# Kernel tuning notes

Hardware: AMD Instinct MI355X
Metric: run time of the kernel (lower is better)

Reference implementation:

```python
import jax, jax.numpy as jnp
import numpy as np

B, N, D, H = 32, 64, 256, 256
WORD_NUM, REL_NUM, POS_NUM, CAT_NUM = 50000, 50, 48, 5


def setup_inputs() -> dict:
    key = jax.random.key(0)
    ks = jax.random.split(key, 20)
    rng = np.random.default_rng(0)
    # valid dependency trees: head[i] < i, head[0] = -1 (root)
    heads_np = np.zeros((B, N), dtype=np.int32)
    for b in range(B):
        heads_np[b, 0] = -1
        for i in range(1, N):
            heads_np[b, i] = rng.integers(0, i)
    p = lambda k, shape: (0.02 * jax.random.normal(k, shape)).astype(jnp.float32)
    z = lambda shape: jnp.zeros(shape, jnp.float32)
    return {
        "xs": jax.random.randint(ks[0], (B, N), 0, WORD_NUM),
        "heads": jnp.asarray(heads_np),
        "rels": jax.random.randint(ks[1], (B, N), 0, REL_NUM),
        "labels": jax.random.randint(ks[2], (B, N), 0, WORD_NUM),
        "poss": jax.random.randint(ks[3], (B, N), 0, POS_NUM),
        "xlengths": jnp.full((B,), N, dtype=jnp.int32),
        "target_start": jnp.zeros((B,), jnp.int32),
        "target_end": jnp.full((B,), N - 1, jnp.int32),
        "x_mask": jnp.ones((B, N), jnp.float32),
        # parameters
        "emb_W": p(ks[4], (WORD_NUM, D)),
        "rel_W": p(ks[5], (REL_NUM, D)),
        "gru_Wi_f": p(ks[6], (2 * D, 3 * H)), "gru_Wh_f": p(ks[7], (H, 3 * H)),
        "gru_bi_f": z((3 * H,)), "gru_bh_f": z((3 * H,)),
        "gru_Wi_b": p(ks[8], (2 * D, 3 * H)), "gru_Wh_b": p(ks[9], (H, 3 * H)),
        "gru_bi_b": z((3 * H,)), "gru_bh_b": z((3 * H,)),
        "Wt": p(ks[10], (2 * H, D)), "bt": z((D,)),
        "dt_Wx": p(ks[11], (2 * D, 3 * H)), "dt_Uh": p(ks[12], (H, 3 * H)), "dt_b": z((3 * H,)),
        "td_Wx": p(ks[13], (2 * D, 3 * H)), "td_Uh": p(ks[14], (H, 3 * H)), "td_b": z((3 * H,)),
        "fc_W": p(ks[15], (2 * H, 100)), "fc_b": z((100,)),
        "fc2_W": p(ks[16], (100, CAT_NUM)), "fc2_b": z((CAT_NUM,)),
    }


def _gru_cell(xpt, hprev, Uh, bh):
    gh = hprev @ Uh + bh
    xr, xz, xn = jnp.split(xpt, 3, axis=-1)
    hr, hz, hn = jnp.split(gh, 3, axis=-1)
    r = jax.nn.sigmoid(xr + hr)
    zg = jax.nn.sigmoid(xz + hz)
    n = jnp.tanh(xn + r * hn)
    return (1.0 - zg) * n + zg * hprev


def _gru_dir(x, Wi, Wh, bi, bh):
    # x: [B,N,2D] -> hidden sequence [B,N,H]
    xp = x @ Wi + bi  # precompute input projections
    def step(h, xpt):
        hnew = _gru_cell(xpt, h, Wh, bh)
        return hnew, hnew
    h0 = jnp.zeros((x.shape[0], Wh.shape[0]), x.dtype)
    _, hs = jax.lax.scan(step, h0, jnp.swapaxes(xp, 0, 1))
    return jnp.swapaxes(hs, 0, 1)


def _dt_tree(inputs, heads, Wx, Uh, b):
    # bottom-up (child-sum) tree GRU; heads[b,i] < i so reversed order is topological
    Bn, Nn, _ = inputs.shape
    Hh = Uh.shape[0]
    xp = inputs @ Wx + b
    bar = jnp.arange(Bn)
    def step(carry, idx):
        C, Hout = carry  # C: accumulated child hidden sums [B,N,H]
        h = _gru_cell(xp[:, idx], C[:, idx], Uh, jnp.zeros((3 * Hh,), inputs.dtype))
        Hout = Hout.at[:, idx].set(h)
        par = heads[:, idx]
        valid = par >= 0
        C = C.at[bar, jnp.where(valid, par, 0)].add(jnp.where(valid[:, None], h, 0.0))
        return (C, Hout), None
    H0 = jnp.zeros((Bn, Nn, Hh), inputs.dtype)
    (_, Hout), _ = jax.lax.scan(step, (H0, H0), jnp.arange(Nn - 1, -1, -1))
    return Hout


def _td_tree(inputs, heads, Wx, Uh, b):
    # top-down tree GRU: parent hidden flows to children; index order 0..N-1 is topological
    Bn, Nn, _ = inputs.shape
    Hh = Uh.shape[0]
    xp = inputs @ Wx + b
    bar = jnp.arange(Bn)
    def step(Hout, idx):
        par = heads[:, idx]
        valid = par >= 0
        hp = jnp.where(valid[:, None], Hout[bar, jnp.where(valid, par, 0)], 0.0)
        h = _gru_cell(xp[:, idx], hp, Uh, jnp.zeros((3 * Hh,), inputs.dtype))
        Hout = Hout.at[:, idx].set(h)
        return Hout, None
    H0 = jnp.zeros((Bn, Nn, Hh), inputs.dtype)
    Hout, _ = jax.lax.scan(step, H0, jnp.arange(Nn))
    return Hout


def reference(xs, heads, rels, labels, poss, xlengths, target_start, target_end, x_mask,
              emb_W, rel_W,
              gru_Wi_f, gru_Wh_f, gru_bi_f, gru_bh_f,
              gru_Wi_b, gru_Wh_b, gru_bi_b, gru_bh_b,
              Wt, bt, dt_Wx, dt_Uh, dt_b, td_Wx, td_Uh, td_b,
              fc_W, fc_b, fc2_W, fc2_b):
    word_emb = emb_W[xs]
    label_emb = emb_W[labels]  # original uses self.embedding for labels too
    emb = jnp.concatenate([word_emb, label_emb], axis=-1)  # [B,N,2D]
    fwd = _gru_dir(emb, gru_Wi_f, gru_Wh_f, gru_bi_f, gru_bh_f)
    bwd = jnp.flip(_gru_dir(jnp.flip(emb, 1), gru_Wi_b, gru_Wh_b, gru_bi_b, gru_bh_b), 1)
    grus = jnp.concatenate([fwd, bwd], axis=-1) @ Wt + bt  # transform -> [B,N,D]
    rel_emb = rel_W[rels]
    outputs = jnp.concatenate([grus, rel_emb], axis=-1)  # [B,N,2D]
    dt_out = _dt_tree(outputs, heads, dt_Wx, dt_Uh, dt_b)
    td_out = _td_tree(outputs, heads, td_Wx, td_Uh, td_b)
    ctx = jnp.concatenate([dt_out, td_out], axis=-1)  # [B,N,2H]
    ctx = jnp.max(ctx, axis=1)  # max_pool1d over length -> [B,2H]
    ctx = ctx @ fc_W + fc_b
    ctx = ctx @ fc2_W + fc2_b
    return ctx
```

## Files before the change

### kernel.cpp

```cpp
#include <hip/hip_runtime.h>


typedef _Float16 half2v __attribute__((ext_vector_type(2)));
typedef _Float16 half8 __attribute__((ext_vector_type(8)));
typedef unsigned int u32x32 __attribute__((ext_vector_type(32)));
typedef float f32x4v __attribute__((ext_vector_type(4)));

__device__ __forceinline__ float fdot2f(unsigned a, unsigned b, float c) {
#if __has_builtin(__builtin_amdgcn_fdot2)
  return __builtin_amdgcn_fdot2(__builtin_bit_cast(half2v, a),
                                __builtin_bit_cast(half2v, b), c, false);
#else
  half2v av = __builtin_bit_cast(half2v, a), bv = __builtin_bit_cast(half2v, b);
  return c + (float)av.x * (float)bv.x + (float)av.y * (float)bv.y;
#endif
}

__device__ __forceinline__ unsigned packh2(float x, float y) {
  half2v p;
  p.x = (_Float16)x;
  p.y = (_Float16)y;
  return __builtin_bit_cast(unsigned, p);
}
__device__ __forceinline__ unsigned short f2u(float x) {
  return __builtin_bit_cast(unsigned short, (_Float16)x);
}
__device__ __forceinline__ float sigm(float x) { return 1.f / (1.f + __expf(-x)); }
__device__ __forceinline__ float tanh_fast(float x) {
  float cx = fminf(fmaxf(x, -15.f), 15.f);
  float e = __expf(2.f * cx);
  return (e - 1.f) / (e + 1.f);
}

__global__ __launch_bounds__(256) void pack_w(const float* __restrict__ W0,
                                              const float* __restrict__ W1,
                                              const float* __restrict__ W2,
                                              const float* __restrict__ W3, unsigned* P0,
                                              unsigned* P1, unsigned* P2, unsigned* P3) {
  const float* W;
  unsigned* P;
  switch (blockIdx.y) {
    case 0: W = W0; P = P0; break;
    case 1: W = W1; P = P1; break;
    case 2: W = W2; P = P2; break;
    default: W = W3; P = P3; break;
  }
  const int tid = blockIdx.x * 256 + threadIdx.x;
  const int i = tid & 3;
  const int u4 = tid >> 2;
  const int jg = u4 & 127;
  const int d4q = u4 >> 7;
  const int d4 = d4q % 48;
  const int q2 = d4q / 48;
  const int col2 = d4 / 24;
  const int rr = d4 % 24;
  const int g = rr >> 3;
  const int p4 = rr & 7;
  const int kp = p4 * 4 + i;
  const int k = q2 * 64 + kp * 2;
  const int col = g * 256 + col2 * 128 + jg;
  P[tid] = packh2(W[(size_t)k * 768 + col], W[(size_t)(k + 1) * 768 + col]);
}

__global__ __launch_bounds__(256) void tsplit2(const float* __restrict__ W0,
                                               const float* __restrict__ W1,
                                               unsigned short* __restrict__ H0,
                                               unsigned short* __restrict__ L0,
                                               unsigned short* __restrict__ H1,
                                               unsigned short* __restrict__ L1, int K,
                                               int N) {
  const float* __restrict__ W = blockIdx.z ? W1 : W0;
  unsigned short* __restrict__ WThi = blockIdx.z ? H1 : H0;
  unsigned short* __restrict__ WTlo = blockIdx.z ? L1 : L0;
  __shared__ float T[32][33];
  const int ky = blockIdx.y * 32, nx = blockIdx.x * 32;
  const int r = threadIdx.x >> 3, c4 = (threadIdx.x & 7) * 4;
  float4 v = *(const float4*)(W + (size_t)(ky + r) * N + nx + c4);
  T[r][c4 + 0] = v.x;
  T[r][c4 + 1] = v.y;
  T[r][c4 + 2] = v.z;
  T[r][c4 + 3] = v.w;
  __syncthreads();
  float f[4] = {T[c4 + 0][r], T[c4 + 1][r], T[c4 + 2][r], T[c4 + 3][r]};
  ushort4 oh, ol;
  {
    _Float16 h0 = (_Float16)f[0], h1 = (_Float16)f[1], h2 = (_Float16)f[2],
             h3 = (_Float16)f[3];
    oh.x = __builtin_bit_cast(unsigned short, h0);
    oh.y = __builtin_bit_cast(unsigned short, h1);
    oh.z = __builtin_bit_cast(unsigned short, h2);
    oh.w = __builtin_bit_cast(unsigned short, h3);
    ol.x = f2u(f[0] - (float)h0);
    ol.y = f2u(f[1] - (float)h1);
    ol.z = f2u(f[2] - (float)h2);
    ol.w = f2u(f[3] - (float)h3);
  }
  *(ushort4*)(WThi + (size_t)(nx + r) * K + ky + c4) = oh;
  *(ushort4*)(WTlo + (size_t)(nx + r) * K + ky + c4) = ol;
}

__global__ void gather_emb_hl(const int* __restrict__ xs, const int* __restrict__ labels,
                              const float* __restrict__ embW,
                              unsigned short* __restrict__ eHi,
                              unsigned short* __restrict__ eLo) {
  const int row = blockIdx.x, t = threadIdx.x;
  const float4* W4 = (const float4*)embW;
  const int src = (t < 64) ? xs[row] : labels[row];
  float4 v = W4[(size_t)src * 64 + (t & 63)];
  float f[4] = {v.x, v.y, v.z, v.w};
  ushort4 oh, ol;
  _Float16 h0 = (_Float16)f[0], h1 = (_Float16)f[1], h2 = (_Float16)f[2],
           h3 = (_Float16)f[3];
  oh.x = __builtin_bit_cast(unsigned short, h0);
  oh.y = __builtin_bit_cast(unsigned short, h1);
  oh.z = __builtin_bit_cast(unsigned short, h2);
// ... 117 lines not shown
        _Float16 h = (_Float16)av[i];
        Ahi[ar][ac8 + i] = h;
        Alo[ar][ac8 + i] = (_Float16)(av[i] - (float)h);
      }
    }
    {
      const float* wp = W + (size_t)(kt + bk) * N + bn + bn8;
      float4 v0 = *(const float4*)wp;
      float4 v1 = *(const float4*)(wp + 4);
      float wv[8] = {v0.x, v0.y, v0.z, v0.w, v1.x, v1.y, v1.z, v1.w};
#pragma unroll
      for (int i = 0; i < 8; ++i) {
        _Float16 h = (_Float16)wv[i];
        Bhi[bn8 + i][bk] = h;
        Blo[bn8 + i][bk] = (_Float16)(wv[i] - (float)h);
      }
    }
    __syncthreads();
    half8 avh = __builtin_bit_cast(half8, *(const uint4*)(&Ahi[fr][fc]));
    half8 avl = __builtin_bit_cast(half8, *(const uint4*)(&Alo[fr][fc]));
#define BH(NT) __builtin_bit_cast(half8, *(const uint4*)(&Bhi[(NT)*16 + lo16][fc]))
#define BL(NT) __builtin_bit_cast(half8, *(const uint4*)(&Blo[(NT)*16 + lo16][fc]))
    half8 b0h = BH(0), b1h = BH(1), b2h = BH(2), b3h = BH(3);
    half8 b0l = BL(0), b1l = BL(1), b2l = BL(2), b3l = BL(3);
#undef BH
#undef BL
    ac0 = __builtin_amdgcn_mfma_f32_16x16x32_f16(avh, b0h, ac0, 0, 0, 0);
    ac1 = __builtin_amdgcn_mfma_f32_16x16x32_f16(avh, b1h, ac1, 0, 0, 0);
    ac2 = __builtin_amdgcn_mfma_f32_16x16x32_f16(avh, b2h, ac2, 0, 0, 0);
    ac3 = __builtin_amdgcn_mfma_f32_16x16x32_f16(avh, b3h, ac3, 0, 0, 0);
    ac0 = __builtin_amdgcn_mfma_f32_16x16x32_f16(avh, b0l, ac0, 0, 0, 0);
    ac1 = __builtin_amdgcn_mfma_f32_16x16x32_f16(avh, b1l, ac1, 0, 0, 0);
    ac2 = __builtin_amdgcn_mfma_f32_16x16x32_f16(avh, b2l, ac2, 0, 0, 0);
    ac3 = __builtin_amdgcn_mfma_f32_16x16x32_f16(avh, b3l, ac3, 0, 0, 0);
    ac0 = __builtin_amdgcn_mfma_f32_16x16x32_f16(avl, b0h, ac0, 0, 0, 0);
    ac1 = __builtin_amdgcn_mfma_f32_16x16x32_f16(avl, b1h, ac1, 0, 0, 0);
    ac2 = __builtin_amdgcn_mfma_f32_16x16x32_f16(avl, b2h, ac2, 0, 0, 0);
    ac3 = __builtin_amdgcn_mfma_f32_16x16x32_f16(avl, b3h, ac3, 0, 0, 0);
    __syncthreads();
  }
  const int hi4 = l >> 4;
#define EPI(AC, NT)                                                            \
  {                                                                            \
    _Pragma("unroll") for (int i = 0; i < 4; ++i) {                            \
      const int row = bm + w * 16 + hi4 * 4 + i;                               \
      const int col = bn + (NT)*16 + lo16;                                     \
      float v = (AC)[i] + bias[col];                                           \
      _Float16 h = (_Float16)v;                                                \
      CHi[(size_t)row * ldc + col] = __builtin_bit_cast(unsigned short, h);    \
      CLo[(size_t)row * ldc + col] = f2u(v - (float)h);                        \
    }                                                                          \
  }
  EPI(ac0, 0) EPI(ac1, 1) EPI(ac2, 2) EPI(ac3, 3)
#undef EPI
}

template <int NP>
__device__ __forceinline__ void stage_w(const uint4* __restrict__ P4, int q2, int jg,
                                        int t, uint2 (*Wl)[512], u32x32& w0, u32x32& w1,
                                        u32x32& w2) {
#pragma unroll
  for (int p4 = 0; p4 < 8; ++p4) {
    uint4 v0 = P4[(q2 * 48 + p4) * 128 + jg];
    w0[4 * p4 + 0] = v0.x; w0[4 * p4 + 1] = v0.y;
    w0[4 * p4 + 2] = v0.z; w0[4 * p4 + 3] = v0.w;
    uint4 v1 = P4[(q2 * 48 + 8 + p4) * 128 + jg];
    w1[4 * p4 + 0] = v1.x; w1[4 * p4 + 1] = v1.y;
    w1[4 * p4 + 2] = v1.z; w1[4 * p4 + 3] = v1.w;
    uint4 v2 = P4[(q2 * 48 + 16 + p4) * 128 + jg];
    w2[4 * p4 + 0] = v2.x; w2[4 * p4 + 1] = v2.y;
    w2[4 * p4 + 2] = v2.z; w2[4 * p4 + 3] = v2.w;
  }
#pragma unroll
  for (int g = 0; g < 3; ++g)
#pragma unroll
    for (int p4 = 0; p4 < NP; ++p4) {
      uint4 v = P4[(q2 * 48 + 24 + g * 8 + p4) * 128 + jg];
      Wl[(g * NP + p4) * 2 + 0][t] = make_uint2(v.x, v.y);
      Wl[(g * NP + p4) * 2 + 1][t] = make_uint2(v.z, v.w);
    }
}

template <int NP>
__device__ __forceinline__ void dot_step(const u32x32& w0, const u32x32& w1,
                                         const u32x32& w2, const uint2 (*Wl)[512], int t,
                                         const uint4* __restrict__ P4, int sb,
                                         const uint4* hv4, float& a0, float& a1,
                                         float& a2, float& a3, float& a4, float& a5) {
#pragma unroll
  for (int c = 0; c < 8; ++c) {
    uint4 hu = hv4[c];
    a0 = fdot2f(w0[4 * c + 0], hu.x, a0); a0 = fdot2f(w0[4 * c + 1], hu.y, a0);
    a0 = fdot2f(w0[4 * c + 2], hu.z, a0); a0 = fdot2f(w0[4 * c + 3], hu.w, a0);
    a1 = fdot2f(w1[4 * c + 0], hu.x, a1); a1 = fdot2f(w1[4 * c + 1], hu.y, a1);
    a1 = fdot2f(w1[4 * c + 2], hu.z, a1); a1 = fdot2f(w1[4 * c + 3], hu.w, a1);
    a2 = fdot2f(w2[4 * c + 0], hu.x, a2); a2 = fdot2f(w2[4 * c + 1], hu.y, a2);
    a2 = fdot2f(w2[4 * c + 2], hu.z, a2); a2 = fdot2f(w2[4 * c + 3], hu.w, a2);
    if (c < NP) {
      uint2 u0 = Wl[(0 * NP + c) * 2 + 0][t], u1 = Wl[(0 * NP + c) * 2 + 1][t];
      a3 = fdot2f(u0.x, hu.x, a3); a3 = fdot2f(u0.y, hu.y, a3);
      a3 = fdot2f(u1.x, hu.z, a3); a3 = fdot2f(u1.y, hu.w, a3);
      uint2 v0 = Wl[(1 * NP + c) * 2 + 0][t], v1 = Wl[(1 * NP + c) * 2 + 1][t];
      a4 = fdot2f(v0.x, hu.x, a4); a4 = fdot2f(v0.y, hu.y, a4);
      a4 = fdot2f(v1.x, hu.z, a4); a4 = fdot2f(v1.y, hu.w, a4);
      uint2 x0 = Wl[(2 * NP + c) * 2 + 0][t], x1 = Wl[(2 * NP + c) * 2 + 1][t];
      a5 = fdot2f(x0.x, hu.x, a5); a5 = fdot2f(x0.y, hu.y, a5);
      a5 = fdot2f(x1.x, hu.z, a5); a5 = fdot2f(x1.y, hu.w, a5);
    } else {
      uint4 s0 = P4[sb + (0 * 8 + c) * 128];
      a3 = fdot2f(s0.x, hu.x, a3); a3 = fdot2f(s0.y, hu.y, a3);
      a3 = fdot2f(s0.z, hu.z, a3); a3 = fdot2f(s0.w, hu.w, a3);
      uint4 s1 = P4[sb + (1 * 8 + c) * 128];
      a4 = fdot2f(s1.x, hu.x, a4); a4 = fdot2f(s1.y, hu.y, a4);
      a4 = fdot2f(s1.z, hu.z, a4); a4 = fdot2f(s1.w, hu.w, a4);
      uint4 s2 = P4[sb + (2 * 8 + c) * 128];
      a5 = fdot2f(s2.x, hu.x, a5); a5 = fdot2f(s2.y, hu.y, a5);
      a5 = fdot2f(s2.z, hu.z, a5); a5 = fdot2f(s2.w, hu.w, a5);
    }
  }
}

__global__ __launch_bounds__(512) void gru_scan_h(
    const unsigned* __restrict__ Pf, const unsigned* __restrict__ Pb,
    const float* __restrict__ bh_f, const float* __restrict__ bh_b,
    const float* __restrict__ xp_f, const float* __restrict__ xp_b,
    float* __restrict__ grus) {
  const int b = blockIdx.x & 31, dir = blockIdx.x >> 5;
  const uint4* __restrict__ P4 = (const uint4*)(dir ? Pb : Pf);
  const float* __restrict__ bh = dir ? bh_b : bh_f;
  const float* __restrict__ xp = dir ? xp_b : xp_f;

  __shared__ uint2 Wl[36][512];
  __shared__ float part[4][3][256];
  __shared__ __align__(16) unsigned h2[128];

  const int t = threadIdx.x, jg = t & 127, q2 = t >> 7;
  const int sb = (q2 * 48 + 24) * 128 + jg;

  u32x32 w0, w1, w2;
  stage_w<6>(P4, q2, jg, t, Wl, w0, w1, w2);

  float br0 = 0.f, br1 = 0.f, bz0 = 0.f, bz1 = 0.f, bn0 = 0.f, bn1 = 0.f;
  float hp0 = 0.f, hp1 = 0.f;
  if (t < 128) {
    br0 = bh[2 * t];       br1 = bh[2 * t + 1];
    bz0 = bh[256 + 2 * t]; bz1 = bh[256 + 2 * t + 1];
    bn0 = bh[512 + 2 * t]; bn1 = bh[512 + 2 * t + 1];
    h2[t] = 0u;
  }
  __syncthreads();

  for (int s = 0; s < 64; ++s) {
    const int nn = dir ? (63 - s) : s;
    float2 pxr, pxz, pxn;
    if (t < 128) {
      const float* xrow = xp + (size_t)(b * 64 + nn) * 768;
      pxr = *(const float2*)(xrow + 2 * t);
      pxz = *(const float2*)(xrow + 256 + 2 * t);
      pxn = *(const float2*)(xrow + 512 + 2 * t);
    }
    float a0 = 0.f, a1 = 0.f, a2 = 0.f, a3 = 0.f, a4 = 0.f, a5 = 0.f;
    dot_step<6>(w0, w1, w2, Wl, t, P4, sb, (const uint4*)(h2 + q2 * 32), a0, a1, a2, a3,
                a4, a5);
    part[q2][0][jg] = a0;
    part[q2][0][128 + jg] = a3;
    part[q2][1][jg] = a1;
    part[q2][1][128 + jg] = a4;
    part[q2][2][jg] = a2;
    part[q2][2][128 + jg] = a5;
    __syncthreads();
    if (t < 128) {
      float s0r = 0, s1r = 0, s0z = 0, s1z = 0, s0n = 0, s1n = 0;
#pragma unroll
      for (int q = 0; q < 4; ++q) {
        float2 pr = *(const float2*)(&part[q][0][2 * t]); s0r += pr.x; s1r += pr.y;
        float2 pz = *(const float2*)(&part[q][1][2 * t]); s0z += pz.x; s1z += pz.y;
        float2 pn = *(const float2*)(&part[q][2][2 * t]); s0n += pn.x; s1n += pn.y;
      }
      float r0 = sigm(pxr.x + s0r + br0), r1 = sigm(pxr.y + s1r + br1);
      float z0 = sigm(pxz.x + s0z + bz0), z1 = sigm(pxz.y + s1z + bz1);
      float n0 = tanh_fast(pxn.x + r0 * (s0n + bn0));
      float n1 = tanh_fast(pxn.y + r1 * (s1n + bn1));
      float h0 = (1.f - z0) * n0 + z0 * hp0;
      float h1 = (1.f - z1) * n1 + z1 * hp1;
      hp0 = h0;
      hp1 = h1;
      h2[t] = packh2(h0, h1);
      float2 o;
      o.x = h0;
      o.y = h1;
      *(float2*)(grus + (size_t)(b * 64 + nn) * 512 + dir * 256 + 2 * t) = o;
    }
    __syncthreads();
  }
}

__global__ __launch_bounds__(512) void tree_scan_g(
    const unsigned* __restrict__ Pdt, const unsigned* __restrict__ Ptd,
    const float* __restrict__ xp_dt, const float* __restrict__ xp_td,
    const int* __restrict__ heads, float* __restrict__ ctx, float* __restrict__ Sg) {
  const int b = blockIdx.x & 31, istd = blockIdx.x >> 5;
  const uint4* __restrict__ P4 = (const uint4*)(istd ? Ptd : Pdt);
  const float* __restrict__ xp = istd ? xp_td : xp_dt;
  float* __restrict__ S = Sg + (size_t)blockIdx.x * 16384;

  __shared__ __align__(16) unsigned S2[65][128];
  __shared__ uint2 Wl[24][512];
  __shared__ float part[4][3][256];
  __shared__ int hd[64];

  const int t = threadIdx.x, jg = t & 127, q2 = t >> 7;
  const int sb = (q2 * 48 + 24) * 128 + jg;

  u32x32 w0, w1, w2;
  stage_w<4>(P4, q2, jg, t, Wl, w0, w1, w2);

  for (int i = t; i < 16384; i += 512) S[i] = 0.f;
  for (int i = t; i < 65 * 128; i += 512) (&S2[0][0])[i] = 0u;
  if (t < 64) hd[t] = heads[b * 64 + t];
  __syncthreads();

  float mx0 = -1e30f, mx1 = -1e30f;

  for (int s = 0; s < 64; ++s) {
    const int idx = istd ? s : (63 - s);
    const int par = hd[idx];
    const int srow = istd ? (par >= 0 ? par : 64) : idx;

    float2 pxr, pxz, pxn;
    float hp0 = 0.f, hp1 = 0.f, acc0 = 0.f, acc1 = 0.f;
    if (t < 128) {
      const float* xrow = xp + (size_t)(b * 64 + idx) * 768;
      pxr = *(const float2*)(xrow + 2 * t);
      pxz = *(const float2*)(xrow + 256 + 2 * t);
      pxn = *(const float2*)(xrow + 512 + 2 * t);
      if (istd) {
        if (par >= 0) {
          float2 v = *(const float2*)(S + par * 256 + 2 * t);
          hp0 = v.x;
          hp1 = v.y;
        }
      } else {
        float2 v = *(const float2*)(S + idx * 256 + 2 * t);
        hp0 = v.x;
        hp1 = v.y;
        if (par >= 0) {
          float2 a = *(const float2*)(S + par * 256 + 2 * t);
          acc0 = a.x;
          acc1 = a.y;
        }
      }
    }
    float a0 = 0.f, a1 = 0.f, a2 = 0.f, a3 = 0.f, a4 = 0.f, a5 = 0.f;
    dot_step<4>(w0, w1, w2, Wl, t, P4, sb, (const uint4*)(&S2[srow][q2 * 32]), a0, a1,
                a2, a3, a4, a5);
    part[q2][0][jg] = a0;
    part[q2][0][128 + jg] = a3;
    part[q2][1][jg] = a1;
    part[q2][1][128 + jg] = a4;
    part[q2][2][jg] = a2;
    part[q2][2][128 + jg] = a5;
    __syncthreads();
    if (t < 128) {
      float s0r = 0, s1r = 0, s0z = 0, s1z = 0, s0n = 0, s1n = 0;
#pragma unroll
      for (int q = 0; q < 4; ++q) {
        float2 pr = *(const float2*)(&part[q][0][2 * t]); s0r += pr.x; s1r += pr.y;
        float2 pz = *(const float2*)(&part[q][1][2 * t]); s0z += pz.x; s1z += pz.y;
        float2 pn = *(const float2*)(&part[q][2][2 * t]); s0n += pn.x; s1n += pn.y;
      }
      float r0 = sigm(pxr.x + s0r), r1 = sigm(pxr.y + s1r);
      float z0 = sigm(pxz.x + s0z), z1 = sigm(pxz.y + s1z);
      float n0 = tanh_fast(pxn.x + r0 * s0n), n1 = tanh_fast(pxn.y + r1 * s1n);
      float h0 = (1.f - z0) * n0 + z0 * hp0;
      float h1 = (1.f - z1) * n1 + z1 * hp1;
      mx0 = fmaxf(mx0, h0);
      mx1 = fmaxf(mx1, h1);
      if (istd) {
        float2 o;
        o.x = h0;
        o.y = h1;
        *(float2*)(S + idx * 256 + 2 * t) = o;
        S2[idx][t] = packh2(h0, h1);
      } else if (par >= 0) {
        float c0 = acc0 + h0;
        float c1 = acc1 + h1;
        float2 o;
        o.x = c0;
        o.y = c1;
        *(float2*)(S + par * 256 + 2 * t) = o;
        S2[par][t] = packh2(c0, c1);
      }
    }
    __syncthreads();
  }

  if (t < 128) {
    float2 o;
    o.x = mx0;
    o.y = mx1;
    *(float2*)(ctx + (size_t)b * 512 + istd * 256 + 2 * t) = o;
  }
}

__global__ __launch_bounds__(128) void final_k(const float* __restrict__ ctx_g,
                                               const float* __restrict__ fcW,
                                               const float* __restrict__ fcb,
                                               const float* __restrict__ fc2W,
                                               const float* __restrict__ fc2b,
                                               float* __restrict__ out) {
  const int b = blockIdx.x, t = threadIdx.x;
  __shared__ float ctx[512];
  __shared__ float f1[100];
  for (int i = t; i < 512; i += 128) ctx[i] = ctx_g[(size_t)b * 512 + i];
  __syncthreads();
  if (t < 100) {
    float a = fcb[t];
    for (int k = 0; k < 512; ++k) a = fmaf(ctx[k], fcW[k * 100 + t], a);
    f1[t] = a;
  }
  __syncthreads();
  if (t < 5) {
    float a = fc2b[t];
    for (int k = 0; k < 100; ++k) a = fmaf(f1[k], fc2W[k * 5 + t], a);
    out[b * 5 + t] = a;
  }
}

extern "C" void kernel_launch(void* const* d_in, const int* in_sizes, int n_in, void* d_out,
                              int out_size, void* d_ws, size_t ws_size, hipStream_t stream) {
  const int* xs = (const int*)d_in[0];
  const int* heads = (const int*)d_in[1];
  const int* rels = (const int*)d_in[2];
  const int* labels = (const int*)d_in[3];
  const float* emb_W = (const float*)d_in[9];
  const float* rel_W = (const float*)d_in[10];
  const float* Wi_f = (const float*)d_in[11];
  const float* Wh_f = (const float*)d_in[12];
  const float* bi_f = (const float*)d_in[13];
  const float* bh_f = (const float*)d_in[14];
  const float* Wi_b = (const float*)d_in[15];
  const float* Wh_b = (const float*)d_in[16];
  const float* bi_b = (const float*)d_in[17];
  const float* bh_b = (const float*)d_in[18];
  const float* Wt = (const float*)d_in[19];
  const float* bt = (const float*)d_in[20];
  const float* dt_Wx = (const float*)d_in[21];
  const float* dt_Uh = (const float*)d_in[22];
  const float* dt_b = (const float*)d_in[23];
  const float* td_Wx = (const float*)d_in[24];
  const float* td_Uh = (const float*)d_in[25];
  const float* td_b = (const float*)d_in[26];
  const float* fc_W = (const float*)d_in[27];
  const float* fc_b = (const float*)d_in[28];
  const float* fc2_W = (const float*)d_in[29];
  const float* fc2_b = (const float*)d_in[30];

  float* ws = (float*)d_ws;
  float* xp_f = ws;
  float* xp_b = ws + 1572864;
  float* grus = ws + 3145728;
  float* ctx = ws + 4194304;
  unsigned* P0 = (unsigned*)(ws + 4210688);
  unsigned* P1 = P0 + 98304;
  unsigned* P2 = P1 + 98304;
  unsigned* P3 = P2 + 98304;
  unsigned short* embHi = (unsigned short*)(ws + 4603904);
  unsigned short* embLo = (unsigned short*)(ws + 5128192);
  unsigned short* WTh_a = (unsigned short*)(ws + 5652480);
  unsigned short* WTl_a = (unsigned short*)(ws + 5849088);
  unsigned short* WTh_b = (unsigned short*)(ws + 6045696);
  unsigned short* WTl_b = (unsigned short*)(ws + 6242304);
  unsigned short* outHi = embHi;
  unsigned short* outLo = embLo;
  float* Sg = ws + 4603904;

  pack_w<<<dim3(384, 4), 256, 0, stream>>>(Wh_f, Wh_b, dt_Uh, td_Uh, P0, P1, P2, P3);
  tsplit2<<<dim3(24, 16, 2), 256, 0, stream>>>(Wi_f, Wi_b, WTh_a, WTl_a, WTh_b, WTl_b,
                                               512, 768);
  gather_emb_hl<<<2048, 128, 0, stream>>>(xs, labels, emb_W, embHi, embLo);
  mm16p<<<dim3(12, 32), 256, 0, stream>>>(embHi, embLo, WTh_a, WTl_a, bi_f, xp_f,
                                          nullptr, nullptr, 768, 0);
  mm16p<<<dim3(12, 32), 256, 0, stream>>>(embHi, embLo, WTh_b, WTl_b, bi_b, xp_b,
                                          nullptr, nullptr, 768, 0);
  gru_scan_h<<<64, 512, 0, stream>>>(P0, P1, bh_f, bh_b, xp_f, xp_b, grus);
  tsplit2<<<dim3(24, 16, 2), 256, 0, stream>>>(dt_Wx, td_Wx, WTh_a, WTl_a, WTh_b, WTl_b,
                                               512, 768);
  mm16s_wt<<<dim3(4, 32), 256, 0, stream>>>(grus, Wt, bt, outHi, outLo, 256, 512);
  gather_rel_hl<<<2048, 64, 0, stream>>>(rels, rel_W, outHi, outLo);
  mm16p<<<dim3(12, 32), 256, 0, stream>>>(outHi, outLo, WTh_a, WTl_a, dt_b, xp_f,
                                          nullptr, nullptr, 768, 0);
  mm16p<<<dim3(12, 32), 256, 0, stream>>>(outHi, outLo, WTh_b, WTl_b, td_b, xp_b,
                                          nullptr, nullptr, 768, 0);
  tree_scan_g<<<64, 512, 0, stream>>>(P2, P3, xp_f, xp_b, heads, ctx, Sg);
  final_k<<<32, 128, 0, stream>>>(ctx, fc_W, fc_b, fc2_W, fc2_b, (float*)d_out);
}
```

Baseline: 325.8 us.

## Process two batch rows per block in GRU and tree scans with shuffle reductions

Each recurrent scan block now handles two batch elements, so every register- or LDS-resident weight load feeds twice as many dot products, and the grid halves from 64 to 32 blocks. The per-step cross-quarter partial-sum reduction moves from a shared-memory buffer plus an extra barrier to wave shuffles, with the thread-to-column mapping reorganised so the four K-quarters sit in one wavefront. GRU hidden state is double-buffered to drop a barrier per step, and tree_scan stages fewer weights in LDS to fit two S2 buffers. The trade-off is fewer blocks on the device and more sequential work per block, and with the new mapping only a quarter of the threads run the gate math.

```diff
diff --git a/kernel.cpp b/kernel.cpp
--- a/kernel.cpp
+++ b/kernel.cpp
@@ -31,6 +31,10 @@
   float e = __expf(2.f * cx);
   return (e - 1.f) / (e + 1.f);
 }
+
+#define RED2(v)                      \
+  v += __shfl_xor(v, 16);            \
+  v += __shfl_xor(v, 32);
 
 __global__ __launch_bounds__(256) void pack_w(const float* __restrict__ W0,
                                               const float* __restrict__ W1,
@@ -314,224 +318,313 @@
 }
 
 template <int NP>
-__device__ __forceinline__ void dot_step(const u32x32& w0, const u32x32& w1,
-                                         const u32x32& w2, const uint2 (*Wl)[512], int t,
-                                         const uint4* __restrict__ P4, int sb,
-                                         const uint4* hv4, float& a0, float& a1,
-                                         float& a2, float& a3, float& a4, float& a5) {
+__device__ __forceinline__ void dot_dual(
+    const u32x32& w0, const u32x32& w1, const u32x32& w2, const uint2 (*Wl)[512], int t,
+    const uint4* __restrict__ P4, int sb, const uint4* hA, const uint4* hB, float& aA0,
+    float& aA1, float& aA2, float& aA3, float& aA4, float& aA5, float& aB0, float& aB1,
+    float& aB2, float& aB3, float& aB4, float& aB5) {
 #pragma unroll
   for (int c = 0; c < 8; ++c) {
-    uint4 hu = hv4[c];
-    a0 = fdot2f(w0[4 * c + 0], hu.x, a0); a0 = fdot2f(w0[4 * c + 1], hu.y, a0);
-    a0 = fdot2f(w0[4 * c + 2], hu.z, a0); a0 = fdot2f(w0[4 * c + 3], hu.w, a0);
-    a1 = fdot2f(w1[4 * c + 0], hu.x, a1); a1 = fdot2f(w1[4 * c + 1], hu.y, a1);
-    a1 = fdot2f(w1[4 * c + 2], hu.z, a1); a1 = fdot2f(w1[4 * c + 3], hu.w, a1);
-    a2 = fdot2f(w2[4 * c + 0], hu.x, a2); a2 = fdot2f(w2[4 * c + 1], hu.y, a2);
-    a2 = fdot2f(w2[4 * c + 2], hu.z, a2); a2 = fdot2f(w2[4 * c + 3], hu.w, a2);
+    uint4 uA = hA[c], uB = hB[c];
+    aA0 = fdot2f(w0[4 * c + 0], uA.x, aA0); aA0 = fdot2f(w0[4 * c + 1], uA.y, aA0);
+    aA0 = fdot2f(w0[4 * c + 2], uA.z, aA0); aA0 = fdot2f(w0[4 * c + 3], uA.w, aA0);
+    aA1 = fdot2f(w1[4 * c + 0], uA.x, aA1); aA1 = fdot2f(w1[4 * c + 1], uA.y, aA1);
+    aA1 = fdot2f(w1[4 * c + 2], uA.z, aA1); aA1 = fdot2f(w1[4 * c + 3], uA.w, aA1);
+    aA2 = fdot2f(w2[4 * c + 0], uA.x, aA2); aA2 = fdot2f(w2[4 * c + 1], uA.y, aA2);
+    aA2 = fdot2f(w2[4 * c + 2], uA.z, aA2); aA2 = fdot2f(w2[4 * c + 3], uA.w, aA2);
+    aB0 = fdot2f(w0[4 * c + 0], uB.x, aB0); aB0 = fdot2f(w0[4 * c + 1], uB.y, aB0);
+    aB0 = fdot2f(w0[4 * c + 2], uB.z, aB0); aB0 = fdot2f(w0[4 * c + 3], uB.w, aB0);
+    aB1 = fdot2f(w1[4 * c + 0], uB.x, aB1); aB1 = fdot2f(w1[4 * c + 1], uB.y, aB1);
+    aB1 = fdot2f(w1[4 * c + 2], uB.z, aB1); aB1 = fdot2f(w1[4 * c + 3], uB.w, aB1);
+    aB2 = fdot2f(w2[4 * c + 0], uB.x, aB2); aB2 = fdot2f(w2[4 * c + 1], uB.y, aB2);
+    aB2 = fdot2f(w2[4 * c + 2], uB.z, aB2); aB2 = fdot2f(w2[4 * c + 3], uB.w, aB2);
     if (c < NP) {
-      uint2 u0 = Wl[(0 * NP + c) * 2 + 0][t], u1 = Wl[(0 * NP + c) * 2 + 1][t];
-      a3 = fdot2f(u0.x, hu.x, a3); a3 = fdot2f(u0.y, hu.y, a3);
-      a3 = fdot2f(u1.x, hu.z, a3); a3 = fdot2f(u1.y, hu.w, a3);
-      uint2 v0 = Wl[(1 * NP + c) * 2 + 0][t], v1 = Wl[(1 * NP + c) * 2 + 1][t];
-      a4 = fdot2f(v0.x, hu.x, a4); a4 = fdot2f(v0.y, hu.y, a4);
-      a4 = fdot2f(v1.x, hu.z, a4); a4 = fdot2f(v1.y, hu.w, a4);
-      uint2 x0 = Wl[(2 * NP + c) * 2 + 0][t], x1 = Wl[(2 * NP + c) * 2 + 1][t];
-      a5 = fdot2f(x0.x, hu.x, a5); a5 = fdot2f(x0.y, hu.y, a5);
-      a5 = fdot2f(x1.x, hu.z, a5); a5 = fdot2f(x1.y, hu.w, a5);
+      {
+        uint2 u0 = Wl[(0 * NP + c) * 2 + 0][t], u1 = Wl[(0 * NP + c) * 2 + 1][t];
+        aA3 = fdot2f(u0.x, uA.x, aA3); aA3 = fdot2f(u0.y, uA.y, aA3);
+        aA3 = fdot2f(u1.x, uA.z, aA3); aA3 = fdot2f(u1.y, uA.w, aA3);
+        aB3 = fdot2f(u0.x, uB.x, aB3); aB3 = fdot2f(u0.y, uB.y, aB3);
+        aB3 = fdot2f(u1.x, uB.z, aB3); aB3 = fdot2f(u1.y, uB.w, aB3);
+      }
+      {
+        uint2 u0 = Wl[(1 * NP + c) * 2 + 0][t], u1 = Wl[(1 * NP + c) * 2 + 1][t];
+        aA4 = fdot2f(u0.x, uA.x, aA4); aA4 = fdot2f(u0.y, uA.y, aA4);
+        aA4 = fdot2f(u1.x, uA.z, aA4); aA4 = fdot2f(u1.y, uA.w, aA4);
+        aB4 = fdot2f(u0.x, uB.x, aB4); aB4 = fdot2f(u0.y, uB.y, aB4);
+        aB4 = fdot2f(u1.x, uB.z, aB4); aB4 = fdot2f(u1.y, uB.w, aB4);
+      }
+      {
+        uint2 u0 = Wl[(2 * NP + c) * 2 + 0][t], u1 = Wl[(2 * NP + c) * 2 + 1][t];
+        aA5 = fdot2f(u0.x, uA.x, aA5); aA5 = fdot2f(u0.y, uA.y, aA5);
+        aA5 = fdot2f(u1.x, uA.z, aA5); aA5 = fdot2f(u1.y, uA.w, aA5);
+        aB5 = fdot2f(u0.x, uB.x, aB5); aB5 = fdot2f(u0.y, uB.y, aB5);
+        aB5 = fdot2f(u1.x, uB.z, aB5); aB5 = fdot2f(u1.y, uB.w, aB5);
+      }
     } else {
       uint4 s0 = P4[sb + (0 * 8 + c) * 128];
-      a3 = fdot2f(s0.x, hu.x, a3); a3 = fdot2f(s0.y, hu.y, a3);
-      a3 = fdot2f(s0.z, hu.z, a3); a3 = fdot2f(s0.w, hu.w, a3);
+      aA3 = fdot2f(s0.x, uA.x, aA3); aA3 = fdot2f(s0.y, uA.y, aA3);
+      aA3 = fdot2f(s0.z, uA.z, aA3); aA3 = fdot2f(s0.w, uA.w, aA3);
+      aB3 = fdot2f(s0.x, uB.x, aB3); aB3 = fdot2f(s0.y, uB.y, aB3);
+      aB3 = fdot2f(s0.z, uB.z, aB3); aB3 = fdot2f(s0.w, uB.w, aB3);
       uint4 s1 = P4[sb + (1 * 8 + c) * 128];
-      a4 = fdot2f(s1.x, hu.x, a4); a4 = fdot2f(s1.y, hu.y, a4);
-      a4 = fdot2f(s1.z, hu.z, a4); a4 = fdot2f(s1.w, hu.w, a4);
+      aA4 = fdot2f(s1.x, uA.x, aA4); aA4 = fdot2f(s1.y, uA.y, aA4);
+      aA4 = fdot2f(s1.z, uA.z, aA4); aA4 = fdot2f(s1.w, uA.w, aA4);
+      aB4 = fdot2f(s1.x, uB.x, aB4); aB4 = fdot2f(s1.y, uB.y, aB4);
+      aB4 = fdot2f(s1.z, uB.z, aB4); aB4 = fdot2f(s1.w, uB.w, aB4);
       uint4 s2 = P4[sb + (2 * 8 + c) * 128];
-      a5 = fdot2f(s2.x, hu.x, a5); a5 = fdot2f(s2.y, hu.y, a5);
-      a5 = fdot2f(s2.z, hu.z, a5); a5 = fdot2f(s2.w, hu.w, a5);
+      aA5 = fdot2f(s2.x, uA.x, aA5); aA5 = fdot2f(s2.y, uA.y, aA5);
+      aA5 = fdot2f(s2.z, uA.z, aA5); aA5 = fdot2f(s2.w, uA.w, aA5);
+      aB5 = fdot2f(s2.x, uB.x, aB5); aB5 = fdot2f(s2.y, uB.y, aB5);
+      aB5 = fdot2f(s2.z, uB.z, aB5); aB5 = fdot2f(s2.w, uB.w, aB5);
     }
   }
 }
 
-__global__ __launch_bounds__(512) void gru_scan_h(
+__global__ __launch_bounds__(512) void gru_scan2(
     const unsigned* __restrict__ Pf, const unsigned* __restrict__ Pb,
     const float* __restrict__ bh_f, const float* __restrict__ bh_b,
     const float* __restrict__ xp_f, const float* __restrict__ xp_b,
     float* __restrict__ grus) {
-  const int b = blockIdx.x & 31, dir = blockIdx.x >> 5;
+  const int blk = blockIdx.x;
+  const int dir = blk >> 4, bp = blk & 15;
+  const int bA = bp, bB = bp + 16;
   const uint4* __restrict__ P4 = (const uint4*)(dir ? Pb : Pf);
   const float* __restrict__ bh = dir ? bh_b : bh_f;
   const float* __restrict__ xp = dir ? xp_b : xp_f;
 
   __shared__ uint2 Wl[36][512];
-  __shared__ float part[4][3][256];
-  __shared__ __align__(16) unsigned h2[128];
-
-  const int t = threadIdx.x, jg = t & 127, q2 = t >> 7;
+  __shared__ __align__(16) unsigned h2A[2][128];
+  __shared__ __align__(16) unsigned h2B[2][128];
+
+  const int t = threadIdx.x;
+  const int lane = t & 63, wv = t >> 6;
+  const int q2 = lane >> 4;
+  const int jg = (lane & 15) + wv * 16;
   const int sb = (q2 * 48 + 24) * 128 + jg;
 
   u32x32 w0, w1, w2;
   stage_w<6>(P4, q2, jg, t, Wl, w0, w1, w2);
 
-  float br0 = 0.f, br1 = 0.f, bz0 = 0.f, bz1 = 0.f, bn0 = 0.f, bn1 = 0.f;
-  float hp0 = 0.f, hp1 = 0.f;
-  if (t < 128) {
-    br0 = bh[2 * t];       br1 = bh[2 * t + 1];
-    bz0 = bh[256 + 2 * t]; bz1 = bh[256 + 2 * t + 1];
-    bn0 = bh[512 + 2 * t]; bn1 = bh[512 + 2 * t + 1];
-    h2[t] = 0u;
+  const bool actv = (q2 == 0);
+  float brl = 0, bzl = 0, bnl = 0, brh = 0, bzh = 0, bnh = 0;
+  float hA0 = 0, hA1 = 0, hB0 = 0, hB1 = 0;
+  if (actv) {
+    brl = bh[jg];       bzl = bh[256 + jg]; bnl = bh[512 + jg];
+    brh = bh[128 + jg]; bzh = bh[384 + jg]; bnh = bh[640 + jg];
+  }
+  if (t < 256) {
+    ((unsigned*)h2A)[t] = 0u;
+    ((unsigned*)h2B)[t] = 0u;
   }
   __syncthreads();
 
   for (int s = 0; s < 64; ++s) {
     const int nn = dir ? (63 - s) : s;
-    float2 pxr, pxz, pxn;
-    if (t < 128) {
-      const float* xrow = xp + (size_t)(b * 64 + nn) * 768;
-      pxr = *(const float2*)(xrow + 2 * t);
-      pxz = *(const float2*)(xrow + 256 + 2 * t);
-      pxn = *(const float2*)(xrow + 512 + 2 * t);
+    const int rb = s & 1, wb2 = rb ^ 1;
+    float xA0, xA1, xA2, xA3, xA4, xA5, xB0, xB1, xB2, xB3, xB4, xB5;
+    if (actv) {
+      const float* xrA = xp + (size_t)(bA * 64 + nn) * 768;
+      const float* xrB = xp + (size_t)(bB * 64 + nn) * 768;
+      xA0 = xrA[jg];       xA1 = xrA[256 + jg]; xA2 = xrA[512 + jg];
+      xA3 = xrA[128 + jg]; xA4 = xrA[384 + jg]; xA5 = xrA[640 + jg];
+      xB0 = xrB[jg];       xB1 = xrB[256 + jg]; xB2 = xrB[512 + jg];
+      xB3 = xrB[128 + jg]; xB4 = xrB[384 + jg]; xB5 = xrB[640 + jg];
     }
-    float a0 = 0.f, a1 = 0.f, a2 = 0.f, a3 = 0.f, a4 = 0.f, a5 = 0.f;
-    dot_step<6>(w0, w1, w2, Wl, t, P4, sb, (const uint4*)(h2 + q2 * 32), a0, a1, a2, a3,
-                a4, a5);
-    part[q2][0][jg] = a0;
-    part[q2][0][128 + jg] = a3;
-    part[q2][1][jg] = a1;
-    part[q2][1][128 + jg] = a4;
-    part[q2][2][jg] = a2;
-    part[q2][2][128 + jg] = a5;
-    __syncthreads();
-    if (t < 128) {
-      float s0r = 0, s1r = 0, s0z = 0, s1z = 0, s0n = 0, s1n = 0;
-#pragma unroll
-      for (int q = 0; q < 4; ++q) {
-        float2 pr = *(const float2*)(&part[q][0][2 * t]); s0r += pr.x; s1r += pr.y;
-        float2 pz = *(const float2*)(&part[q][1][2 * t]); s0z += pz.x; s1z += pz.y;
-        float2 pn = *(const float2*)(&part[q][2][2 * t]); s0n += pn.x; s1n += pn.y;
-      }
-      float r0 = sigm(pxr.x + s0r + br0), r1 = sigm(pxr.y + s1r + br1);
-      float z0 = sigm(pxz.x + s0z + bz0), z1 = sigm(pxz.y + s1z + bz1);
-      float n0 = tanh_fast(pxn.x + r0 * (s0n + bn0));
-      float n1 = tanh_fast(pxn.y + r1 * (s1n + bn1));
-      float h0 = (1.f - z0) * n0 + z0 * hp0;
-      float h1 = (1.f - z1) * n1 + z1 * hp1;
-      hp0 = h0;
-      hp1 = h1;
-      h2[t] = packh2(h0, h1);
-      float2 o;
-      o.x = h0;
-      o.y = h1;
-      *(float2*)(grus + (size_t)(b * 64 + nn) * 512 + dir * 256 + 2 * t) = o;
+    float aA0 = 0, aA1 = 0, aA2 = 0, aA3 = 0, aA4 = 0, aA5 = 0;
+    float aB0 = 0, aB1 = 0, aB2 = 0, aB3 = 0, aB4 = 0, aB5 = 0;
+    dot_dual<6>(w0, w1, w2, Wl, t, P4, sb, (const uint4*)(&h2A[rb][q2 * 32]),
+                (const uint4*)(&h2B[rb][q2 * 32]), aA0, aA1, aA2, aA3, aA4, aA5, aB0,
+                aB1, aB2, aB3, aB4, aB5);
+    RED2(aA0) RED2(aA1) RED2(aA2) RED2(aA3) RED2(aA4) RED2(aA5)
+    RED2(aB0) RED2(aB1) RED2(aB2) RED2(aB3) RED2(aB4) RED2(aB5)
+    if (actv) {
+      {
+        float r = sigm(xA0 + aA0 + brl), z = sigm(xA1 + aA1 + bzl);
+        float n = tanh_fast(xA2 + r * (aA2 + bnl));
+        hA0 = (1.f - z) * n + z * hA0;
+      }
+      {
+        float r = sigm(xA3 + aA3 + brh), z = sigm(xA4 + aA4 + bzh);
+        float n = tanh_fast(xA5 + r * (aA5 + bnh));
+        hA1 = (1.f - z) * n + z * hA1;
+      }
+      {
+        float r = sigm(xB0 + aB0 + brl), z = sigm(xB1 + aB1 + bzl);
+        float n = tanh_fast(xB2 + r * (aB2 + bnl));
+        hB0 = (1.f - z) * n + z * hB0;
+      }
+      {
+        float r = sigm(xB3 + aB3 + brh), z = sigm(xB4 + aB4 + bzh);
+        float n = tanh_fast(xB5 + r * (aB5 + bnh));
+        hB1 = (1.f - z) * n + z * hB1;
+      }
+      grus[(size_t)(bA * 64 + nn) * 512 + dir * 256 + jg] = hA0;
+      grus[(size_t)(bA * 64 + nn) * 512 + dir * 256 + 128 + jg] = hA1;
+      grus[(size_t)(bB * 64 + nn) * 512 + dir * 256 + jg] = hB0;
+      grus[(size_t)(bB * 64 + nn) * 512 + dir * 256 + 128 + jg] = hB1;
+      float pA0 = __shfl_xor(hA0, 1), pA1 = __shfl_xor(hA1, 1);
+      float pB0 = __shfl_xor(hB0, 1), pB1 = __shfl_xor(hB1, 1);
+      if ((jg & 1) == 0) {
+        h2A[wb2][jg >> 1] = packh2(hA0, pA0);
+        h2A[wb2][64 + (jg >> 1)] = packh2(hA1, pA1);
+        h2B[wb2][jg >> 1] = packh2(hB0, pB0);
+        h2B[wb2][64 + (jg >> 1)] = packh2(hB1, pB1);
+      }
     }
     __syncthreads();
   }
 }
 
-__global__ __launch_bounds__(512) void tree_scan_g(
+__global__ __launch_bounds__(512) void tree_scan2(
     const unsigned* __restrict__ Pdt, const unsigned* __restrict__ Ptd,
     const float* __restrict__ xp_dt, const float* __restrict__ xp_td,
     const int* __restrict__ heads, float* __restrict__ ctx, float* __restrict__ Sg) {
-  const int b = blockIdx.x & 31, istd = blockIdx.x >> 5;
+  const int blk = blockIdx.x;
+  const int istd = blk >> 4, bp = blk & 15;
+  const int bA = bp, bB = bp + 16;
   const uint4* __restrict__ P4 = (const uint4*)(istd ? Ptd : Pdt);
   const float* __restrict__ xp = istd ? xp_td : xp_dt;
-  float* __restrict__ S = Sg + (size_t)blockIdx.x * 16384;
-
-  __shared__ __align__(16) unsigned S2[65][128];
-  __shared__ uint2 Wl[24][512];
-  __shared__ float part[4][3][256];
-  __shared__ int hd[64];
-
-  const int t = threadIdx.x, jg = t & 127, q2 = t >> 7;
+  float* __restrict__ SA = Sg + (size_t)(blk * 2 + 0) * 16384;
+  float* __restrict__ SB = Sg + (size_t)(blk * 2 + 1) * 16384;
+
+  __shared__ uint2 Wl[18][512];
+  __shared__ __align__(16) unsigned S2A[64][128];
+  __shared__ __align__(16) unsigned S2B[64][128];
+  __shared__ int hdA[64], hdB[64];
+
+  const int t = threadIdx.x;
+  const int lane = t & 63, wv = t >> 6;
+  const int q2 = lane >> 4;
+  const int jg = (lane & 15) + wv * 16;
   const int sb = (q2 * 48 + 24) * 128 + jg;
 
   u32x32 w0, w1, w2;
-  stage_w<4>(P4, q2, jg, t, Wl, w0, w1, w2);
-
-  for (int i = t; i < 16384; i += 512) S[i] = 0.f;
-  for (int i = t; i < 65 * 128; i += 512) (&S2[0][0])[i] = 0u;
-  if (t < 64) hd[t] = heads[b * 64 + t];
+  stage_w<3>(P4, q2, jg, t, Wl, w0, w1, w2);
+
+  for (int i = t; i < 16384; i += 512) {
+    SA[i] = 0.f;
+    SB[i] = 0.f;
+  }
+  for (int i = t; i < 8192; i += 512) {
+    ((unsigned*)S2A)[i] = 0u;
+    ((unsigned*)S2B)[i] = 0u;
+  }
+  if (t < 64) {
+    hdA[t] = heads[bA * 64 + t];
+    hdB[t] = heads[bB * 64 + t];
+  }
   __syncthreads();
 
-  float mx0 = -1e30f, mx1 = -1e30f;
+  const bool actv = (q2 == 0);
+  float mxA0 = -1e30f, mxA1 = -1e30f, mxB0 = -1e30f, mxB1 = -1e30f;
 
   for (int s = 0; s < 64; ++s) {
     const int idx = istd ? s : (63 - s);
-    const int par = hd[idx];
-    const int srow = istd ? (par >= 0 ? par : 64) : idx;
-
-    float2 pxr, pxz, pxn;
-    float hp0 = 0.f, hp1 = 0.f, acc0 = 0.f, acc1 = 0.f;
-    if (t < 128) {
-      const float* xrow = xp + (size_t)(b * 64 + idx) * 768;
-      pxr = *(const float2*)(xrow + 2 * t);
-      pxz = *(const float2*)(xrow + 256 + 2 * t);
-      pxn = *(const float2*)(xrow + 512 + 2 * t);
+    const int parA = hdA[idx], parB = hdB[idx];
+    const int srowA = istd ? (parA >= 0 ? parA : 0) : idx;
+    const int srowB = istd ? (parB >= 0 ? parB : 0) : idx;
+
+    float xA0, xA1, xA2, xA3, xA4, xA5, xB0, xB1, xB2, xB3, xB4, xB5;
+    float hpA0 = 0, hpA1 = 0, hpB0 = 0, hpB1 = 0;
+    float acA0 = 0, acA1 = 0, acB0 = 0, acB1 = 0;
+    if (actv) {
+      const float* xrA = xp + (size_t)(bA * 64 + idx) * 768;
+      const float* xrB = xp + (size_t)(bB * 64 + idx) * 768;
+      xA0 = xrA[jg];       xA1 = xrA[256 + jg]; xA2 = xrA[512 + jg];
+      xA3 = xrA[128 + jg]; xA4 = xrA[384 + jg]; xA5 = xrA[640 + jg];
+      xB0 = xrB[jg];       xB1 = xrB[256 + jg]; xB2 = xrB[512 + jg];
+      xB3 = xrB[128 + jg]; xB4 = xrB[384 + jg]; xB5 = xrB[640 + jg];
       if (istd) {
-        if (par >= 0) {
-          float2 v = *(const float2*)(S + par * 256 + 2 * t);
-          hp0 = v.x;
-          hp1 = v.y;
+        if (parA >= 0) { hpA0 = SA[parA * 256 + jg]; hpA1 = SA[parA * 256 + 128 + jg]; }
+        if (parB >= 0) { hpB0 = SB[parB * 256 + jg]; hpB1 = SB[parB * 256 + 128 + jg]; }
+      } else {
+        hpA0 = SA[idx * 256 + jg];
+        hpA1 = SA[idx * 256 + 128 + jg];
+        hpB0 = SB[idx * 256 + jg];
+        hpB1 = SB[idx * 256 + 128 + jg];
+        if (parA >= 0) { acA0 = SA[parA * 256 + jg]; acA1 = SA[parA * 256 + 128 + jg]; }
+        if (parB >= 0) { acB0 = SB[parB * 256 + jg]; acB1 = SB[parB * 256 + 128 + jg]; }
+      }
+    }
+    float aA0 = 0, aA1 = 0, aA2 = 0, aA3 = 0, aA4 = 0, aA5 = 0;
+    float aB0 = 0, aB1 = 0, aB2 = 0, aB3 = 0, aB4 = 0, aB5 = 0;
+    dot_dual<3>(w0, w1, w2, Wl, t, P4, sb, (const uint4*)(&S2A[srowA][q2 * 32]),
+                (const uint4*)(&S2B[srowB][q2 * 32]), aA0, aA1, aA2, aA3, aA4, aA5, aB0,
+                aB1, aB2, aB3, aB4, aB5);
+    RED2(aA0) RED2(aA1) RED2(aA2) RED2(aA3) RED2(aA4) RED2(aA5)
+    RED2(aB0) RED2(aB1) RED2(aB2) RED2(aB3) RED2(aB4) RED2(aB5)
+    if (actv) {
+      float hA0, hA1, hB0, hB1;
+      {
+        float r = sigm(xA0 + aA0), z = sigm(xA1 + aA1);
+        float n = tanh_fast(xA2 + r * aA2);
+        hA0 = (1.f - z) * n + z * hpA0;
+      }
+      {
+        float r = sigm(xA3 + aA3), z = sigm(xA4 + aA4);
+        float n = tanh_fast(xA5 + r * aA5);
+        hA1 = (1.f - z) * n + z * hpA1;
+      }
+      {
+        float r = sigm(xB0 + aB0), z = sigm(xB1 + aB1);
+        float n = tanh_fast(xB2 + r * aB2);
+        hB0 = (1.f - z) * n + z * hpB0;
+      }
+      {
+        float r = sigm(xB3 + aB3), z = sigm(xB4 + aB4);
+        float n = tanh_fast(xB5 + r * aB5);
+        hB1 = (1.f - z) * n + z * hpB1;
+      }
+      mxA0 = fmaxf(mxA0, hA0);
+      mxA1 = fmaxf(mxA1, hA1);
+      mxB0 = fmaxf(mxB0, hB0);
+      mxB1 = fmaxf(mxB1, hB1);
+      if (istd) {
+        SA[idx * 256 + jg] = hA0;
+        SA[idx * 256 + 128 + jg] = hA1;
+        SB[idx * 256 + jg] = hB0;
+        SB[idx * 256 + 128 + jg] = hB1;
+        float pA0 = __shfl_xor(hA0, 1), pA1 = __shfl_xor(hA1, 1);
+        float pB0 = __shfl_xor(hB0, 1), pB1 = __shfl_xor(hB1, 1);
+        if ((jg & 1) == 0) {
+          S2A[idx][jg >> 1] = packh2(hA0, pA0);
+          S2A[idx][64 + (jg >> 1)] = packh2(hA1, pA1);
+          S2B[idx][jg >> 1] = packh2(hB0, pB0);
+          S2B[idx][64 + (jg >> 1)] = packh2(hB1, pB1);
         }
       } else {
-        float2 v = *(const float2*)(S + idx * 256 + 2 * t);
-        hp0 = v.x;
-        hp1 = v.y;
-        if (par >= 0) {
-          float2 a = *(const float2*)(S + par * 256 + 2 * t);
-          acc0 = a.x;
-          acc1 = a.y;
+        float cA0 = acA0 + hA0, cA1 = acA1 + hA1;
+        float cB0 = acB0 + hB0, cB1 = acB1 + hB1;
+        if (parA >= 0) {
+          SA[parA * 256 + jg] = cA0;
+          SA[parA * 256 + 128 + jg] = cA1;
         }
-      }
-    }
-    float a0 = 0.f, a1 = 0.f, a2 = 0.f, a3 = 0.f, a4 = 0.f, a5 = 0.f;
-    dot_step<4>(w0, w1, w2, Wl, t, P4, sb, (const uint4*)(&S2[srow][q2 * 32]), a0, a1,
-                a2, a3, a4, a5);
-    part[q2][0][jg] = a0;
-    part[q2][0][128 + jg] = a3;
-    part[q2][1][jg] = a1;
-    part[q2][1][128 + jg] = a4;
-    part[q2][2][jg] = a2;
-    part[q2][2][128 + jg] = a5;
-    __syncthreads();
-    if (t < 128) {
-      float s0r = 0, s1r = 0, s0z = 0, s1z = 0, s0n = 0, s1n = 0;
-#pragma unroll
-      for (int q = 0; q < 4; ++q) {
-        float2 pr = *(const float2*)(&part[q][0][2 * t]); s0r += pr.x; s1r += pr.y;
-        float2 pz = *(const float2*)(&part[q][1][2 * t]); s0z += pz.x; s1z += pz.y;
-        float2 pn = *(const float2*)(&part[q][2][2 * t]); s0n += pn.x; s1n += pn.y;
-      }
-      float r0 = sigm(pxr.x + s0r), r1 = sigm(pxr.y + s1r);
-      float z0 = sigm(pxz.x + s0z), z1 = sigm(pxz.y + s1z);
-      float n0 = tanh_fast(pxn.x + r0 * s0n), n1 = tanh_fast(pxn.y + r1 * s1n);
-      float h0 = (1.f - z0) * n0 + z0 * hp0;
-      float h1 = (1.f - z1) * n1 + z1 * hp1;
-      mx0 = fmaxf(mx0, h0);
-      mx1 = fmaxf(mx1, h1);
-      if (istd) {
-        float2 o;
-        o.x = h0;
-        o.y = h1;
-        *(float2*)(S + idx * 256 + 2 * t) = o;
-        S2[idx][t] = packh2(h0, h1);
-      } else if (par >= 0) {
-        float c0 = acc0 + h0;
-        float c1 = acc1 + h1;
-        float2 o;
-        o.x = c0;
-        o.y = c1;
-        *(float2*)(S + par * 256 + 2 * t) = o;
-        S2[par][t] = packh2(c0, c1);
+        if (parB >= 0) {
+          SB[parB * 256 + jg] = cB0;
+          SB[parB * 256 + 128 + jg] = cB1;
+        }
+        float pA0 = __shfl_xor(cA0, 1), pA1 = __shfl_xor(cA1, 1);
+        float pB0 = __shfl_xor(cB0, 1), pB1 = __shfl_xor(cB1, 1);
+        if ((jg & 1) == 0) {
+          if (parA >= 0) {
+            S2A[parA][jg >> 1] = packh2(cA0, pA0);
+            S2A[parA][64 + (jg >> 1)] = packh2(cA1, pA1);
+          }
+          if (parB >= 0) {
+            S2B[parB][jg >> 1] = packh2(cB0, pB0);
+            S2B[parB][64 + (jg >> 1)] = packh2(cB1, pB1);
+          }
+        }
       }
     }
     __syncthreads();
   }
 
-  if (t < 128) {
-    float2 o;
-    o.x = mx0;
-    o.y = mx1;
-    *(float2*)(ctx + (size_t)b * 512 + istd * 256 + 2 * t) = o;
+  if (actv) {
+    ctx[(size_t)bA * 512 + istd * 256 + jg] = mxA0;
+    ctx[(size_t)bA * 512 + istd * 256 + 128 + jg] = mxA1;
+    ctx[(size_t)bB * 512 + istd * 256 + jg] = mxB0;
+    ctx[(size_t)bB * 512 + istd * 256 + 128 + jg] = mxB1;
   }
 }
 
@@ -615,7 +708,7 @@
                                           nullptr, nullptr, 768, 0);
   mm16p<<<dim3(12, 32), 256, 0, stream>>>(embHi, embLo, WTh_b, WTl_b, bi_b, xp_b,
                                           nullptr, nullptr, 768, 0);
-  gru_scan_h<<<64, 512, 0, stream>>>(P0, P1, bh_f, bh_b, xp_f, xp_b, grus);
+  gru_scan2<<<32, 512, 0, stream>>>(P0, P1, bh_f, bh_b, xp_f, xp_b, grus);
   tsplit2<<<dim3(24, 16, 2), 256, 0, stream>>>(dt_Wx, td_Wx, WTh_a, WTl_a, WTh_b, WTl_b,
                                                512, 768);
   mm16s_wt<<<dim3(4, 32), 256, 0, stream>>>(grus, Wt, bt, outHi, outLo, 256, 512);
@@ -624,6 +717,6 @@
                                           nullptr, nullptr, 768, 0);
   mm16p<<<dim3(12, 32), 256, 0, stream>>>(outHi, outLo, WTh_b, WTl_b, td_b, xp_b,
                                           nullptr, nullptr, 768, 0);
-  tree_scan_g<<<64, 512, 0, stream>>>(P2, P3, xp_f, xp_b, heads, ctx, Sg);
+  tree_scan2<<<32, 512, 0, stream>>>(P2, P3, xp_f, xp_b, heads, ctx, Sg);
   final_k<<<32, 128, 0, stream>>>(ctx, fc_W, fc_b, fc2_W, fc2_b, (float*)d_out);
 }
```

Result: slower. 569.1 us (+74.7%).
